# Kernel tuning notes

Measured on AMD Instinct MI355X. Metric: run time of the kernel, lower is better.

The kernel has to match this reference:

```python
import jax, jax.numpy as jnp
import numpy as np

B, C, H, W = 2, 512, 48, 48
HEADS, DHEAD = 8, 64
INNER = HEADS * DHEAD  # 512
CTX_LEN, CTX_DIM = 77, 768
FF_INNER = 4 * INNER   # 2048 (GEGLU inner dim)
GN_GROUPS, GN_EPS, LN_EPS = 32, 1e-6, 1e-5
SCALE = DHEAD ** -0.5


def setup_inputs() -> dict:
    key = jax.random.key(0)
    ks = iter(jax.random.split(key, 32))
    def nrm(shape, s=0.02):
        return jax.random.normal(next(ks), shape, jnp.float32) * s
    return dict(
        x=jax.random.normal(next(ks), (B, C, H, W), jnp.float32),
        context=jax.random.normal(next(ks), (B, CTX_LEN, CTX_DIM), jnp.float32),
        gn_g=jnp.ones((C,), jnp.float32), gn_b=jnp.zeros((C,), jnp.float32),
        w_in=nrm((C, INNER)), b_in=jnp.zeros((INNER,), jnp.float32),
        ln1_g=jnp.ones((INNER,), jnp.float32), ln1_b=jnp.zeros((INNER,), jnp.float32),
        wq1=nrm((INNER, INNER)), wk1=nrm((INNER, INNER)), wv1=nrm((INNER, INNER)),
        wo1=nrm((INNER, INNER)), bo1=jnp.zeros((INNER,), jnp.float32),
        ln2_g=jnp.ones((INNER,), jnp.float32), ln2_b=jnp.zeros((INNER,), jnp.float32),
        wq2=nrm((INNER, INNER)), wk2=nrm((CTX_DIM, INNER)), wv2=nrm((CTX_DIM, INNER)),
        wo2=nrm((INNER, INNER)), bo2=jnp.zeros((INNER,), jnp.float32),
        ln3_g=jnp.ones((INNER,), jnp.float32), ln3_b=jnp.zeros((INNER,), jnp.float32),
        w_ff1=nrm((INNER, 2 * FF_INNER)), b_ff1=jnp.zeros((2 * FF_INNER,), jnp.float32),
        w_ff2=nrm((FF_INNER, INNER)), b_ff2=jnp.zeros((INNER,), jnp.float32),
        w_out=nrm((INNER, C)), b_out=jnp.zeros((C,), jnp.float32),
    )


def _layernorm(x, g, b):
    m = jnp.mean(x, -1, keepdims=True)
    v = jnp.var(x, -1, keepdims=True)
    return (x - m) * jax.lax.rsqrt(v + LN_EPS) * g + b


def _groupnorm(x, g, b):
    bs, c, h, w = x.shape
    xg = x.reshape(bs, GN_GROUPS, c // GN_GROUPS, h, w)
    m = jnp.mean(xg, (2, 3, 4), keepdims=True)
    v = jnp.var(xg, (2, 3, 4), keepdims=True)
    xg = (xg - m) * jax.lax.rsqrt(v + GN_EPS)
    return xg.reshape(bs, c, h, w) * g[None, :, None, None] + b[None, :, None, None]


def _attn(x, ctx, wq, wk, wv, wo, bo):
    bs, n, _ = x.shape
    m = ctx.shape[1]
    q = (x @ wq).reshape(bs, n, HEADS, DHEAD).transpose(0, 2, 1, 3)    # b h n d
    k = (ctx @ wk).reshape(bs, m, HEADS, DHEAD).transpose(0, 2, 1, 3)  # b h m d
    v = (ctx @ wv).reshape(bs, m, HEADS, DHEAD).transpose(0, 2, 1, 3)
    sim = jnp.einsum('bhid,bhjd->bhij', q, k) * SCALE
    a = jax.nn.softmax(sim, axis=-1)
    o = jnp.einsum('bhij,bhjd->bhid', a, v)
    o = o.transpose(0, 2, 1, 3).reshape(bs, n, INNER)
    return o @ wo + bo


def reference(x, context, gn_g, gn_b, w_in, b_in,
              ln1_g, ln1_b, wq1, wk1, wv1, wo1, bo1,
              ln2_g, ln2_b, wq2, wk2, wv2, wo2, bo2,
              ln3_g, ln3_b, w_ff1, b_ff1, w_ff2, b_ff2,
              w_out, b_out):
    x_in = x
    h = _groupnorm(x, gn_g, gn_b)
    # proj_in: 1x1 conv == channel-wise linear
    h = jnp.einsum('bchw,cd->bdhw', h, w_in) + b_in[None, :, None, None]
    t = h.reshape(B, INNER, H * W).transpose(0, 2, 1)  # b n c
    # BasicTransformerBlock (depth=1)
    hn = _layernorm(t, ln1_g, ln1_b)
    t = _attn(hn, hn, wq1, wk1, wv1, wo1, bo1) + t          # self-attention
    hn = _layernorm(t, ln2_g, ln2_b)
    t = _attn(hn, context, wq2, wk2, wv2, wo2, bo2) + t     # cross-attention
    hn = _layernorm(t, ln3_g, ln3_b)
    u = hn @ w_ff1 + b_ff1                                   # GEGLU proj
    a_, g_ = jnp.split(u, 2, axis=-1)
    t = (a_ * jax.nn.gelu(g_, approximate=False)) @ w_ff2 + b_ff2 + t
    # back to image + proj_out 1x1 conv + residual
    y = t.transpose(0, 2, 1).reshape(B, INNER, H, W)
    y = jnp.einsum('bchw,cd->bdhw', y, w_out) + b_out[None, :, None, None]
    return y + x_in
```

## Files before the change

### kernel.cpp

```cpp
#include <hip/hip_runtime.h>
#include <hip/hip_bf16.h>

typedef __bf16 bf16_t;
typedef __bf16 bf16x4 __attribute__((ext_vector_type(4)));
typedef __bf16 bf16x8 __attribute__((ext_vector_type(8)));
typedef float f32x4 __attribute__((ext_vector_type(4)));

static __device__ __forceinline__ bf16x8 bzero8() {
  bf16x8 v;
#pragma unroll
  for (int j = 0; j < 8; j++) v[j] = (bf16_t)0.f;
  return v;
}

static __device__ __forceinline__ void async_copy16(const bf16_t* g, bf16_t* l) {
  __builtin_amdgcn_global_load_lds((const __attribute__((address_space(1))) void*)g,
                                   (__attribute__((address_space(3))) void*)l,
                                   16, 0, 0);
}
#define WAVE_LGKM() asm volatile("s_waitcnt lgkmcnt(0)" ::: "memory")

static __device__ __forceinline__ float fast_exp2(float x) {
  float r;
  asm volatile("v_exp_f32 %0, %1" : "=v"(r) : "v"(x));
  return r;
}

#define QK_SCALE 0.18033688f

__global__ void probe_kernel(const void* x, int* flag) {
  if (threadIdx.x != 0 || blockIdx.x != 0) return;
  const unsigned short* u = (const unsigned short*)x;
  int insane = 0;
  for (int j = 0; j < 512; j++) {
    unsigned short h = u[j];
    int e = (h >> 7) & 0xFF;
    if (e == 0xFF || e > 140 || (e != 0 && e < 100)) insane++;
  }
  *flag = (insane > 16) ? 1 : 0;
}

struct ConvArgs { const void* src[28]; int n[28]; int off[28]; };
__global__ __launch_bounds__(256) void convert_kernel(ConvArgs a, const int* flag,
                                                      bf16_t* dst) {
  int i = blockIdx.y;
  if (i >= 28) return;
  int n = a.n[i];
  if (n == 0) return;
  const void* s = a.src[i];
  bf16_t* d = dst + a.off[i];
  bool f32 = (*flag != 0);
  int n4 = n >> 2;
  for (int j = blockIdx.x * 256 + threadIdx.x; j < n4; j += gridDim.x * 256) {
    bf16x4 o;
    if (f32) {
      float4 v = ((const float4*)s)[j];
      o[0] = (bf16_t)v.x; o[1] = (bf16_t)v.y; o[2] = (bf16_t)v.z; o[3] = (bf16_t)v.w;
    } else {
      o = ((const bf16x4*)s)[j];
    }
    ((bf16x4*)d)[j] = o;
  }
  int base = n4 << 2;
  int j = base + blockIdx.x * 256 + threadIdx.x;
  if (j < n) {
    float v = f32 ? ((const float*)s)[j] : (float)((const bf16_t*)s)[j];
    d[j] = (bf16_t)v;
  }
}

struct TransArgs { const void* src[10]; int dst_off[10]; int K[10]; int N[10]; };
__global__ __launch_bounds__(256) void transpose_kernel(TransArgs ta, const int* flag,
                                                        bf16_t* __restrict__ wt) {
  int wi = blockIdx.y;
  int K = ta.K[wi], N = ta.N[wi];
  int tiles_n = N >> 6;
  int tile = blockIdx.x;
  if (tile >= tiles_n * (K >> 6)) return;
  int tk = tile / tiles_n, tn = tile - tk * tiles_n;
  int k0 = tk * 64, n0 = tn * 64;
  bf16_t* dst = wt + ta.dst_off[wi];
  bool f32 = (*flag != 0);
  __shared__ bf16_t tl[64][66];
  int t = threadIdx.x;
  int r = t >> 2, c = (t & 3) * 16;
  if (f32) {
    const float* src = (const float*)ta.src[wi] + (size_t)(k0 + r) * N + n0 + c;
#pragma unroll
    for (int q = 0; q < 4; q++) {
      float4 v = *(const float4*)(src + q * 4);
      tl[r][c + q * 4 + 0] = (bf16_t)v.x;
      tl[r][c + q * 4 + 1] = (bf16_t)v.y;
      tl[r][c + q * 4 + 2] = (bf16_t)v.z;
      tl[r][c + q * 4 + 3] = (bf16_t)v.w;
    }
  } else {
    const bf16_t* src = (const bf16_t*)ta.src[wi] + (size_t)(k0 + r) * N + n0 + c;
    bf16x8 v0 = *(const bf16x8*)(src);
    bf16x8 v1 = *(const bf16x8*)(src + 8);
#pragma unroll
    for (int j = 0; j < 8; j++) { tl[r][c + j] = v0[j]; tl[r][c + 8 + j] = v1[j]; }
  }
  __syncthreads();
  bf16x8 o0, o1;
#pragma unroll
  for (int j = 0; j < 8; j++) { o0[j] = tl[c + j][r]; o1[j] = tl[c + 8 + j][r]; }
  *(bf16x8*)(dst + (size_t)(n0 + r) * K + k0 + c) = o0;
  *(bf16x8*)(dst + (size_t)(n0 + r) * K + k0 + c + 8) = o1;
}

__global__ __launch_bounds__(256) void gn_stats_kernel(const bf16_t* __restrict__ x,
                                                       float* __restrict__ stats) {
  const bf16x8* base = (const bf16x8*)(x + (size_t)blockIdx.x * 36864);
  float s = 0.f, ss = 0.f;
  for (int i = threadIdx.x; i < 4608; i += 256) {
    bf16x8 v = base[i];
#pragma unroll
    for (int j = 0; j < 8; j++) { float f = (float)v[j]; s += f; ss += f * f; }
  }
  __shared__ float red[8];
#pragma unroll
  for (int off = 32; off > 0; off >>= 1) { s += __shfl_down(s, off); ss += __shfl_down(ss, off); }
  int wid = threadIdx.x >> 6;
  if ((threadIdx.x & 63) == 0) { red[wid] = s; red[4 + wid] = ss; }
  __syncthreads();
  if (threadIdx.x == 0) {
    float S = red[0] + red[1] + red[2] + red[3];
    float SS = red[4] + red[5] + red[6] + red[7];
    const float inv = 1.0f / 36864.0f;
    float mean = S * inv;
    float var = SS * inv - mean * mean;
    stats[blockIdx.x * 2] = mean;
    stats[blockIdx.x * 2 + 1] = rsqrtf(fmaxf(var, 0.f) + 1e-6f);
  }
}

__global__ __launch_bounds__(256) void gn_apply_kernel(const bf16_t* __restrict__ x,
                                                       const float* __restrict__ stats,
                                                       const bf16_t* __restrict__ g,
                                                       const bf16_t* __restrict__ bb,
                                                       bf16_t* __restrict__ xnt) {
  int p0 = blockIdx.x * 64, c0 = blockIdx.y * 64, bz = blockIdx.z;
  __shared__ bf16_t tl[64][66];
  int t = threadIdx.x;
  int r = t >> 2, cc = (t & 3) * 16;
  int c = c0 + r;
  float mean = stats[(bz * 32 + (c >> 4)) * 2];
  float rstd = stats[(bz * 32 + (c >> 4)) * 2 + 1];
  float gg = (float)g[c], bbv = (float)bb[c];
  const bf16_t* row = x + ((size_t)(bz * 512 + c)) * 2304 + p0 + cc;
  bf16x8 v0 = *(const bf16x8*)(row);
  bf16x8 v1 = *(const bf16x8*)(row + 8);
#pragma unroll
  for (int j = 0; j < 8; j++) {
    tl[r][cc + j] = (bf16_t)(((float)v0[j] - mean) * rstd * gg + bbv);
    tl[r][cc + 8 + j] = (bf16_t)(((float)v1[j] - mean) * rstd * gg + bbv);
  }
  __syncthreads();
  bf16x8 o0, o1;
#pragma unroll
  for (int j = 0; j < 8; j++) { o0[j] = tl[cc + j][r]; o1[j] = tl[cc + 8 + j][r]; }
  bf16_t* orow = xnt + ((size_t)(bz * 2304 + p0 + r)) * 512 + c0 + cc;
  *(bf16x8*)(orow) = o0;
  *(bf16x8*)(orow + 8) = o1;
}

__global__ __launch_bounds__(256) void ln_kernel(const float* __restrict__ in,
                                                 const bf16_t* __restrict__ g,
                                                 const bf16_t* __restrict__ b,
                                                 bf16_t* __restrict__ out) {
  int tok = blockIdx.x * 4 + (threadIdx.x >> 6);
  int lane = threadIdx.x & 63;
  const float* row = in + (size_t)tok * 512 + lane * 8;
  float f[8];
  float s = 0.f, ss = 0.f;
#pragma unroll
  for (int j = 0; j < 8; j++) { f[j] = row[j]; s += f[j]; ss += f[j] * f[j]; }
#pragma unroll
  for (int off = 32; off > 0; off >>= 1) { s += __shfl_xor(s, off); ss += __shfl_xor(ss, off); }
  float mean = s * (1.0f / 512.0f);
  float var = ss * (1.0f / 512.0f) - mean * mean;
  float rstd = rsqrtf(fmaxf(var, 0.f) + 1e-5f);
  bf16x8 gv = *(const bf16x8*)(g + lane * 8);
  bf16x8 bv = *(const bf16x8*)(b + lane * 8);
  bf16x8 o;
#pragma unroll
  for (int j = 0; j < 8; j++) o[j] = (bf16_t)((f[j] - mean) * rstd * (float)gv[j] + (float)bv[j]);
  *(bf16x8*)(out + (size_t)tok * 512 + lane * 8) = o;
}

template <int SMODE, int MODE>
__global__ __launch_bounds__(256) void gemm64d_kernel(
    const bf16_t* __restrict__ A, int lda,
    const bf16_t* __restrict__ Bt, int K, int N,
    const bf16_t* __restrict__ bias, float oscale,
    float* __restrict__ t32, bf16_t* __restrict__ C,
    const bf16_t* __restrict__ resb, const float* __restrict__ resf,
    float* __restrict__ Cf, const int* dflag) {
  __shared__ bf16_t As[2][4096];
  __shared__ bf16_t Bs[2][4096];
  int t = threadIdx.x, w = t >> 6, quad = (t >> 4) & 3, l16 = t & 15;
  int m0 = blockIdx.y * 64, n0 = blockIdx.x * 64;
  int wm = (w >> 1) * 32, wn = (w & 1) * 32;
  const f32x4 z4 = {0.f, 0.f, 0.f, 0.f};
  f32x4 acc[2][2] = {{z4, z4}, {z4, z4}};
  int r0 = t >> 3, c0 = ((t & 7) ^ (r0 & 7)) * 8;
  int r1 = r0 + 32, c1 = ((t & 7) ^ (r1 & 7)) * 8;
  const bf16_t* Ar0 = A + (size_t)(m0 + r0) * lda + c0;
  const bf16_t* Ar1 = A + (size_t)(m0 + r1) * lda + c1;
  const bf16_t* Br0 = Bt + (size_t)(n0 + r0) * K + c0;
  const bf16_t* Br1 = Bt + (size_t)(n0 + r1) * K + c1;
  int niter = K >> 6;
  async_copy16(Ar0, As[0] + w * 512);
  async_copy16(Ar1, As[0] + 2048 + w * 512);
  async_copy16(Br0, Bs[0] + w * 512);
  async_copy16(Br1, Bs[0] + 2048 + w * 512);
  for (int it = 0; it < niter; it++) {
    __syncthreads();
    if (it + 1 < niter) {
      int k0 = (it + 1) << 6;
      int nb = (it + 1) & 1;
      async_copy16(Ar0 + k0, As[nb] + w * 512);
      async_copy16(Ar1 + k0, As[nb] + 2048 + w * 512);
      async_copy16(Br0 + k0, Bs[nb] + w * 512);
      async_copy16(Br1 + k0, Bs[nb] + 2048 + w * 512);
    }
    int cb = it & 1;
    bf16x8 af[2][2], bff[2][2];
#pragma unroll
    for (int mi = 0; mi < 2; mi++) {
      int rr = wm + mi * 16 + l16;
      af[mi][0] = *(const bf16x8*)&As[cb][(rr * 8 + (quad ^ (rr & 7))) * 8];
      af[mi][1] = *(const bf16x8*)&As[cb][(rr * 8 + ((quad + 4) ^ (rr & 7))) * 8];
    }
#pragma unroll
    for (int ni = 0; ni < 2; ni++) {
      int rr = wn + ni * 16 + l16;
      bff[ni][0] = *(const bf16x8*)&Bs[cb][(rr * 8 + (quad ^ (rr & 7))) * 8];
      bff[ni][1] = *(const bf16x8*)&Bs[cb][(rr * 8 + ((quad + 4) ^ (rr & 7))) * 8];
    }
#pragma unroll
    for (int mi = 0; mi < 2; mi++)
#pragma unroll
      for (int ni = 0; ni < 2; ni++) {
        acc[mi][ni] = __builtin_amdgcn_mfma_f32_16x16x32_bf16(af[mi][0], bff[ni][0], acc[mi][ni], 0, 0, 0);
        acc[mi][ni] = __builtin_amdgcn_mfma_f32_16x16x32_bf16(af[mi][1], bff[ni][1], acc[mi][ni], 0, 0, 0);
      }
  }
  const bool f32m = (MODE == 3) && (*dflag != 0);
#pragma unroll
  for (int mi = 0; mi < 2; mi++)
#pragma unroll
    for (int ni = 0; ni < 2; ni++) {
      int col = n0 + wn + ni * 16 + l16;
      float bv = bias ? (float)bias[col] : 0.f;
#pragma unroll
      for (int r = 0; r < 4; r++) {
        int row = m0 + wm + mi * 16 + quad * 4 + r;
        float v = acc[mi][ni][r] + bv;
        size_t addr;
        if (SMODE == 0) {
          addr = (size_t)row * N + col;
        } else {
          int b2 = row / 2304; int p = row - b2 * 2304;
          addr = ((size_t)(b2 * 512 + col)) * 2304 + p;
        }
        if (MODE == 0) C[addr] = (bf16_t)(v * oscale);
        else if (MODE == 1) { t32[addr] = v; C[addr] = (bf16_t)v; }
        else if (MODE == 2) { v += t32[addr]; t32[addr] = v; C[addr] = (bf16_t)v; }
        else {
          v += f32m ? resf[addr] : (float)resb[addr];
          if (f32m) Cf[addr] = v; else C[addr] = (bf16_t)v;
        }
      }
    }
}

__global__ __launch_bounds__(256) void qkv3_kernel(
    const bf16_t* __restrict__ A,
    const bf16_t* __restrict__ BtQ, const bf16_t* __restrict__ BtK,
    const bf16_t* __restrict__ BtV,
    bf16_t* __restrict__ Qo, bf16_t* __restrict__ Ko, bf16_t* __restrict__ Vt) {
  __shared__ bf16_t As[2][4096];
  __shared__ bf16_t Bs[3][2][4096];
  int t = threadIdx.x, w = t >> 6, quad = (t >> 4) & 3, l16 = t & 15;
  int m0 = blockIdx.y * 64, n0 = blockIdx.x * 64;
  int wm = (w >> 1) * 32, wn = (w & 1) * 32;
  const f32x4 z4 = {0.f, 0.f, 0.f, 0.f};
  f32x4 acc[3][2][2];
#pragma unroll
  for (int z = 0; z < 3; z++)
#pragma unroll
    for (int mi = 0; mi < 2; mi++)
#pragma unroll
      for (int ni = 0; ni < 2; ni++) acc[z][mi][ni] = z4;
  int r0 = t >> 3, c0 = ((t & 7) ^ (r0 & 7)) * 8;
  int r1 = r0 + 32, c1 = ((t & 7) ^ (r1 & 7)) * 8;
  const bf16_t* Ar0 = A + (size_t)(m0 + r0) * 512 + c0;
  const bf16_t* Ar1 = A + (size_t)(m0 + r1) * 512 + c1;
  const bf16_t* Bw[3] = {BtQ, BtK, BtV};
  const bf16_t* Br0[3];
  const bf16_t* Br1[3];
#pragma unroll
  for (int z = 0; z < 3; z++) {
    Br0[z] = Bw[z] + (size_t)(n0 + r0) * 512 + c0;
    Br1[z] = Bw[z] + (size_t)(n0 + r1) * 512 + c1;
  }
  async_copy16(Ar0, As[0] + w * 512);
  async_copy16(Ar1, As[0] + 2048 + w * 512);
#pragma unroll
  for (int z = 0; z < 3; z++) {
    async_copy16(Br0[z], Bs[z][0] + w * 512);
    async_copy16(Br1[z], Bs[z][0] + 2048 + w * 512);
  }
  for (int it = 0; it < 8; it++) {
    __syncthreads();
    if (it + 1 < 8) {
      int k0 = (it + 1) << 6;
      int nb = (it + 1) & 1;
      async_copy16(Ar0 + k0, As[nb] + w * 512);
      async_copy16(Ar1 + k0, As[nb] + 2048 + w * 512);
#pragma unroll
      for (int z = 0; z < 3; z++) {
        async_copy16(Br0[z] + k0, Bs[z][nb] + w * 512);
        async_copy16(Br1[z] + k0, Bs[z][nb] + 2048 + w * 512);
      }
    }
    int cb = it & 1;
    bf16x8 af[2][2];
#pragma unroll
    for (int mi = 0; mi < 2; mi++) {
      int rr = wm + mi * 16 + l16;
      af[mi][0] = *(const bf16x8*)&As[cb][(rr * 8 + (quad ^ (rr & 7))) * 8];
      af[mi][1] = *(const bf16x8*)&As[cb][(rr * 8 + ((quad + 4) ^ (rr & 7))) * 8];
    }
#pragma unroll
    for (int z = 0; z < 3; z++) {
      bf16x8 bff[2][2];
#pragma unroll
      for (int ni = 0; ni < 2; ni++) {
        int rr = wn + ni * 16 + l16;
        bff[ni][0] = *(const bf16x8*)&Bs[z][cb][(rr * 8 + (quad ^ (rr & 7))) * 8];
        bff[ni][1] = *(const bf16x8*)&Bs[z][cb][(rr * 8 + ((quad + 4) ^ (rr & 7))) * 8];
      }
#pragma unroll
      for (int mi = 0; mi < 2; mi++)
#pragma unroll
        for (int ni = 0; ni < 2; ni++) {
          acc[z][mi][ni] = __builtin_amdgcn_mfma_f32_16x16x32_bf16(af[mi][0], bff[ni][0], acc[z][mi][ni], 0, 0, 0);
          acc[z][mi][ni] = __builtin_amdgcn_mfma_f32_16x16x32_bf16(af[mi][1], bff[ni][1], acc[z][mi][ni], 0, 0, 0);
        }
    }
  }
#pragma unroll
  for (int mi = 0; mi < 2; mi++)
#pragma unroll
    for (int ni = 0; ni < 2; ni++) {
      int col = n0 + wn + ni * 16 + l16;
#pragma unroll
      for (int r = 0; r < 4; r++) {
        int row = m0 + wm + mi * 16 + quad * 4 + r;
        Qo[(size_t)row * 512 + col] = (bf16_t)(acc[0][mi][ni][r] * QK_SCALE);
        Ko[(size_t)row * 512 + col] = (bf16_t)acc[1][mi][ni][r];
        int b2 = row / 2304; int p = row - b2 * 2304;
        Vt[((size_t)(b2 * 512 + col)) * 2304 + p] = (bf16_t)acc[2][mi][ni][r];
      }
    }
}

__global__ __launch_bounds__(256) void ff1_kernel(const bf16_t* __restrict__ A,
                                                  const bf16_t* __restrict__ Bt,
                                                  const bf16_t* __restrict__ bias,
                                                  bf16_t* __restrict__ U) {
  __shared__ bf16_t As[2][4096];
  __shared__ bf16_t Ba[2][4096];
  __shared__ bf16_t Bg[2][4096];
  int t = threadIdx.x, w = t >> 6, quad = (t >> 4) & 3, l16 = t & 15;
  int m0 = blockIdx.y * 64, n0 = blockIdx.x * 64;
  int wm = (w >> 1) * 32, wn = (w & 1) * 32;
  const f32x4 z4 = {0.f, 0.f, 0.f, 0.f};
  f32x4 aa[2][2] = {{z4, z4}, {z4, z4}};
  f32x4 ag[2][2] = {{z4, z4}, {z4, z4}};
  int r0 = t >> 3, c0 = ((t & 7) ^ (r0 & 7)) * 8;
  int r1 = r0 + 32, c1 = ((t & 7) ^ (r1 & 7)) * 8;
  const bf16_t* Ar0 = A + (size_t)(m0 + r0) * 512 + c0;
  const bf16_t* Ar1 = A + (size_t)(m0 + r1) * 512 + c1;
  const bf16_t* Ba0 = Bt + (size_t)(n0 + r0) * 512 + c0;
  const bf16_t* Ba1 = Bt + (size_t)(n0 + r1) * 512 + c1;
  const bf16_t* Bg0 = Bt + (size_t)(2048 + n0 + r0) * 512 + c0;
  const bf16_t* Bg1 = Bt + (size_t)(2048 + n0 + r1) * 512 + c1;
  async_copy16(Ar0, As[0] + w * 512);
  async_copy16(Ar1, As[0] + 2048 + w * 512);
  async_copy16(Ba0, Ba[0] + w * 512);
  async_copy16(Ba1, Ba[0] + 2048 + w * 512);
  async_copy16(Bg0, Bg[0] + w * 512);
  async_copy16(Bg1, Bg[0] + 2048 + w * 512);
  for (int it = 0; it < 8; it++) {
    __syncthreads();
    if (it + 1 < 8) {
      int k0 = (it + 1) << 6;
      int nb = (it + 1) & 1;
      async_copy16(Ar0 + k0, As[nb] + w * 512);
      async_copy16(Ar1 + k0, As[nb] + 2048 + w * 512);
      async_copy16(Ba0 + k0, Ba[nb] + w * 512);
      async_copy16(Ba1 + k0, Ba[nb] + 2048 + w * 512);
      async_copy16(Bg0 + k0, Bg[nb] + w * 512);
      async_copy16(Bg1 + k0, Bg[nb] + 2048 + w * 512);
    }
    int cb = it & 1;
    bf16x8 af[2][2], ba[2][2], bg[2][2];
#pragma unroll
    for (int mi = 0; mi < 2; mi++) {
      int rr = wm + mi * 16 + l16;
      af[mi][0] = *(const bf16x8*)&As[cb][(rr * 8 + (quad ^ (rr & 7))) * 8];
      af[mi][1] = *(const bf16x8*)&As[cb][(rr * 8 + ((quad + 4) ^ (rr & 7))) * 8];
    }
#pragma unroll
    for (int ni = 0; ni < 2; ni++) {
      int rr = wn + ni * 16 + l16;
      int o0 = (rr * 8 + (quad ^ (rr & 7))) * 8;
      int o1 = (rr * 8 + ((quad + 4) ^ (rr & 7))) * 8;
      ba[ni][0] = *(const bf16x8*)&Ba[cb][o0];
      ba[ni][1] = *(const bf16x8*)&Ba[cb][o1];
      bg[ni][0] = *(const bf16x8*)&Bg[cb][o0];
      bg[ni][1] = *(const bf16x8*)&Bg[cb][o1];
    }
#pragma unroll
    for (int mi = 0; mi < 2; mi++)
#pragma unroll
      for (int ni = 0; ni < 2; ni++) {
        aa[mi][ni] = __builtin_amdgcn_mfma_f32_16x16x32_bf16(af[mi][0], ba[ni][0], aa[mi][ni], 0, 0, 0);
        aa[mi][ni] = __builtin_amdgcn_mfma_f32_16x16x32_bf16(af[mi][1], ba[ni][1], aa[mi][ni], 0, 0, 0);
        ag[mi][ni] = __builtin_amdgcn_mfma_f32_16x16x32_bf16(af[mi][0], bg[ni][0], ag[mi][ni], 0, 0, 0);
        ag[mi][ni] = __builtin_amdgcn_mfma_f32_16x16x32_bf16(af[mi][1], bg[ni][1], ag[mi][ni], 0, 0, 0);
      }
  }
#pragma unroll
  for (int mi = 0; mi < 2; mi++)
#pragma unroll
    for (int ni = 0; ni < 2; ni++) {
      int col = n0 + wn + ni * 16 + l16;
      float bba = (float)bias[col], bbg = (float)bias[col + 2048];
#pragma unroll
      for (int r = 0; r < 4; r++) {
        int row = m0 + wm + mi * 16 + quad * 4 + r;
        float a = aa[mi][ni][r] + bba;
        float g = ag[mi][ni][r] + bbg;
        float gl = 0.5f * g * (1.0f + erff(g * 0.70710678118654752f));
        U[(size_t)row * 2048 + col] = (bf16_t)(a * gl);
      }
    }
}

__global__ __launch_bounds__(256) void kv2_kernel(const bf16_t* __restrict__ A,
                                                  const bf16_t* __restrict__ Bk,
                                                  const bf16_t* __restrict__ Bv,
                                                  bf16_t* __restrict__ Ck,
                                                  bf16_t* __restrict__ Cv) {
  const int M = 154, N = 512, K = 768;
  int z = blockIdx.z;
  const bf16_t* B = z ? Bv : Bk;
  __shared__ alignas(16) bf16_t As[64][40];
  __shared__ alignas(16) bf16_t Bs[64][40];
  int t = threadIdx.x;
  int m0 = blockIdx.y * 64, n0 = blockIdx.x * 64;
  int w = t >> 6, lane = t & 63, quad = lane >> 4, l16 = lane & 15;
  int ar = t >> 2, ac = (t & 3) * 8;
  int br = t >> 3, bc = (t & 7) * 8;
  const f32x4 z4 = {0.f, 0.f, 0.f, 0.f};
  f32x4 acc[4] = {z4, z4, z4, z4};
  int gm = m0 + ar;
  const bool a_ok = gm < M;
  for (int k0 = 0; k0 < K; k0 += 32) {
    bf16x8 av = a_ok ? *(const bf16x8*)(A + (size_t)gm * K + k0 + ac) : bzero8();
    bf16x8 bv = *(const bf16x8*)(B + (size_t)(k0 + br) * N + n0 + bc);
    __syncthreads();
    *(bf16x8*)(&As[ar][ac]) = av;
#pragma unroll
    for (int j = 0; j < 8; j++) Bs[bc + j][br] = bv[j];
    __syncthreads();
    bf16x8 afrag = *(const bf16x8*)(&As[w * 16 + l16][quad * 8]);
#pragma unroll
    for (int kb = 0; kb < 4; kb++) {
      bf16x8 bfrag = *(const bf16x8*)(&Bs[kb * 16 + l16][quad * 8]);
      acc[kb] = __builtin_amdgcn_mfma_f32_16x16x32_bf16(afrag, bfrag, acc[kb], 0, 0, 0);
    }
  }
#pragma unroll
  for (int kb = 0; kb < 4; kb++) {
    int col = n0 + kb * 16 + l16;
#pragma unroll
    for (int r = 0; r < 4; r++) {
      int row = m0 + w * 16 + quad * 4 + r;
      if (row < M) {
        float v = acc[kb][r];
        if (z == 0) Ck[(size_t)row * N + col] = (bf16_t)v;
        else {
          int b2 = row / 77; int p = row - b2 * 77;
          Cv[((size_t)(b2 * 512 + col)) * 128 + p] = (bf16_t)v;
        }
      }
    }
  }
}

template <bool MASK>
__global__ __launch_bounds__(128) void flash6_kernel(const bf16_t* __restrict__ q,
                                                     const bf16_t* __restrict__ kk,
                                                     const bf16_t* __restrict__ vt,
                                                     bf16_t* __restrict__ out,
                                                     int n_k, int kv_bstride, int vt_len) {
  __shared__ bf16_t Ks[2][4096];
  __shared__ bf16_t Vs[2][4096];
  __shared__ bf16_t p_lds[2][32 * 72];
  int t = threadIdx.x, w = t >> 6, quad = (t >> 4) & 3, l16 = t & 15;
  int b = blockIdx.y >> 3, h = blockIdx.y & 7;
  int q0 = blockIdx.x * 64 + w * 32;
  bf16x8 qa[2][2];
#pragma unroll
  for (int si = 0; si < 2; si++) {
    const bf16_t* qrow = q + ((size_t)(b * 2304 + q0 + si * 16 + l16)) * 512 + h * 64 + quad * 8;
    qa[si][0] = *(const bf16x8*)(qrow);
    qa[si][1] = *(const bf16x8*)(qrow + 32);
  }
  const f32x4 z4 = {0.f, 0.f, 0.f, 0.f};
  f32x4 o[2][4];
  float l_i[2] = {0.f, 0.f};
#pragma unroll
  for (int si = 0; si < 2; si++)
#pragma unroll
    for (int db = 0; db < 4; db++) o[si][db] = z4;
  const bf16_t* kbase = kk + (size_t)b * kv_bstride + h * 64;
  const bf16_t* vbase = vt + ((size_t)((b * 8 + h) * 64)) * vt_len;
  int kr[4], kc[4];
#pragma unroll
  for (int i = 0; i < 4; i++) {
    int g = t + 128 * i;
    kr[i] = g >> 3;
    kc[i] = ((g & 7) ^ (kr[i] & 7)) * 8;
  }
  int n_kt = (n_k + 63) >> 6;
#pragma unroll
  for (int i = 0; i < 4; i++) {
    async_copy16(kbase + (size_t)kr[i] * 512 + kc[i], Ks[0] + w * 512 + i * 1024);
    async_copy16(vbase + (size_t)kr[i] * vt_len + kc[i], Vs[0] + w * 512 + i * 1024);
  }
  for (int kt = 0; kt < n_kt; kt++) {
    int kc0 = kt * 64;
    __syncthreads();
    if (kt + 1 < n_kt) {
      int kn = (kt + 1) * 64;
      int nb = (kt + 1) & 1;
#pragma unroll
      for (int i = 0; i < 4; i++) {
        async_copy16(kbase + (size_t)(kn + kr[i]) * 512 + kc[i], Ks[nb] + w * 512 + i * 1024);
        async_copy16(vbase + (size_t)kr[i] * vt_len + kn + kc[i], Vs[nb] + w * 512 + i * 1024);
      }
    }
    int cb = kt & 1;
    bf16x8 kf[4][2], vf[4][2];
#pragma unroll
    for (int kb = 0; kb < 4; kb++) {
      int rr = kb * 16 + l16;
#pragma unroll
      for (int c = 0; c < 2; c++) {
        int gi = (rr * 8 + ((quad + c * 4) ^ (rr & 7))) * 8;
        kf[kb][c] = *(const bf16x8*)&Ks[cb][gi];
        vf[kb][c] = *(const bf16x8*)&Vs[cb][gi];
      }
    }
#pragma unroll
    for (int si = 0; si < 2; si++) {
      f32x4 s[4] = {z4, z4, z4, z4};
#pragma unroll
      for (int kb = 0; kb < 4; kb++) {
        s[kb] = __builtin_amdgcn_mfma_f32_16x16x32_bf16(kf[kb][0], qa[si][0], s[kb], 0, 0, 0);
        s[kb] = __builtin_amdgcn_mfma_f32_16x16x32_bf16(kf[kb][1], qa[si][1], s[kb], 0, 0, 0);
      }
      float rs = 0.f;
#pragma unroll
      for (int kb = 0; kb < 4; kb++)
#pragma unroll
        for (int r = 0; r < 4; r++) {
          float sv = s[kb][r];
          if (MASK && (kc0 + kb * 16 + quad * 4 + r) >= n_k) sv = -1e30f;
          float pp = fast_exp2(sv);
          s[kb][r] = pp;
          rs += pp;
        }
      rs += __shfl_xor(rs, 16);
      rs += __shfl_xor(rs, 32);
      l_i[si] += rs;
      WAVE_LGKM();
#pragma unroll
      for (int kb = 0; kb < 4; kb++) {
        bf16x4 pk;
#pragma unroll
        for (int r = 0; r < 4; r++) pk[r] = (bf16_t)s[kb][r];
        *(bf16x4*)&p_lds[w][(si * 16 + l16) * 72 + kb * 16 + quad * 4] = pk;
      }
      WAVE_LGKM();
      bf16x8 pa0 = *(const bf16x8*)&p_lds[w][(si * 16 + l16) * 72 + quad * 8];
      bf16x8 pa1 = *(const bf16x8*)&p_lds[w][(si * 16 + l16) * 72 + 32 + quad * 8];
#pragma unroll
      for (int db = 0; db < 4; db++) {
        o[si][db] = __builtin_amdgcn_mfma_f32_16x16x32_bf16(vf[db][0], pa0, o[si][db], 0, 0, 0);
        o[si][db] = __builtin_amdgcn_mfma_f32_16x16x32_bf16(vf[db][1], pa1, o[si][db], 0, 0, 0);
      }
    }
  }
#pragma unroll
  for (int si = 0; si < 2; si++) {
    float inv = 1.0f / l_i[si];
    bf16_t* orow = out + ((size_t)(b * 2304 + q0 + si * 16 + l16)) * 512 + h * 64 + quad * 4;
#pragma unroll
    for (int db = 0; db < 4; db++) {
      bf16x4 pk;
#pragma unroll
      for (int r = 0; r < 4; r++) pk[r] = (bf16_t)(o[si][db][r] * inv);
      *(bf16x4*)(orow + db * 16) = pk;
    }
  }
}

extern "C" void kernel_launch(void* const* d_in, const int* in_sizes, int n_in,
                              void* d_out, int out_size, void* d_ws, size_t ws_size,
                              hipStream_t stream) {
  (void)out_size; (void)ws_size;
  char* p = (char*)d_ws;
  int* flag = (int*)p;
  float* stats = (float*)(p + 16);
  float* t32 = (float*)(p + 1024);
  const size_t TOK512 = (size_t)4608 * 512;
  bf16_t* conv = (bf16_t*)(p + 1024 + TOK512 * 4);

  const int widx[10] = {4, 8, 9, 10, 11, 15, 18, 22, 24, 26};
  const int wK[10] = {512, 512, 512, 512, 512, 512, 512, 512, 2048, 512};
  const int wN[10] = {512, 512, 512, 512, 512, 512, 512, 4096, 512, 512};
  bool is_wt[28] = {};
  for (int i = 0; i < 10; i++) is_wt[widx[i]] = true;

  ConvArgs ca;
  int off = 0;
  int noff[28];
  for (int i = 0; i < 28; i++) {
    ca.src[i] = (i < n_in) ? d_in[i] : nullptr;
    ca.n[i] = (i < n_in && !is_wt[i]) ? in_sizes[i] : 0;
    ca.off[i] = off;
    noff[i] = off;
    int sz = (i < n_in) ? in_sizes[i] : 0;
    off += ((is_wt[i] ? 0 : sz) + 7) & ~7;
  }
  bf16_t* wt = conv + ((off + 7) & ~7);
  TransArgs ta;
  int woff = 0, wtoff[10];
  for (int i = 0; i < 10; i++) {
    ta.src[i] = d_in[widx[i]];
    ta.dst_off[i] = woff;
    wtoff[i] = woff;
    ta.K[i] = wK[i]; ta.N[i] = wN[i];
    woff += wK[i] * wN[i];
  }
  bf16_t* hn  = wt + woff;
  bf16_t* tb  = hn + TOK512;
  bf16_t* xnt = tb + TOK512;
  bf16_t* qb  = xnt + TOK512;
  bf16_t* kbuf = qb + TOK512;
  bf16_t* vtb = kbuf + TOK512;
  bf16_t* ub2 = xnt;
  bf16_t* ob  = xnt;

  const bf16_t* xb    = conv + noff[0];
  const bf16_t* ctxb  = conv + noff[1];
  const bf16_t* gn_g  = conv + noff[2];
  const bf16_t* gn_b  = conv + noff[3];
  const bf16_t* b_in  = conv + noff[5];
  const bf16_t* ln1_g = conv + noff[6];
  const bf16_t* ln1_b = conv + noff[7];
  const bf16_t* bo1   = conv + noff[12];
  const bf16_t* ln2_g = conv + noff[13];
  const bf16_t* ln2_b = conv + noff[14];
  const bf16_t* wk2   = conv + noff[16];
  const bf16_t* wv2   = conv + noff[17];
  const bf16_t* bo2   = conv + noff[19];
  const bf16_t* ln3_g = conv + noff[20];
  const bf16_t* ln3_b = conv + noff[21];
  const bf16_t* b_ff1 = conv + noff[23];
  const bf16_t* b_ff2 = conv + noff[25];
  const bf16_t* b_out = conv + noff[27];
  const bf16_t* wt_in  = wt + wtoff[0];
  const bf16_t* wt_q1  = wt + wtoff[1];
  const bf16_t* wt_k1  = wt + wtoff[2];
  const bf16_t* wt_v1  = wt + wtoff[3];
  const bf16_t* wt_o1  = wt + wtoff[4];
  const bf16_t* wt_q2  = wt + wtoff[5];
  const bf16_t* wt_o2  = wt + wtoff[6];
  const bf16_t* wt_ff1 = wt + wtoff[7];
  const bf16_t* wt_ff2 = wt + wtoff[8];
  const bf16_t* wt_out = wt + wtoff[9];

  probe_kernel<<<1, 64, 0, stream>>>(d_in[0], flag);
  convert_kernel<<<dim3(128, 28), 256, 0, stream>>>(ca, flag, conv);
  transpose_kernel<<<dim3(512, 10), 256, 0, stream>>>(ta, flag, wt);

  gn_stats_kernel<<<64, 256, 0, stream>>>(xb, stats);
  gn_apply_kernel<<<dim3(36, 8, 2), 256, 0, stream>>>(xb, stats, gn_g, gn_b, xnt);
  gemm64d_kernel<0, 1><<<dim3(8, 72), 256, 0, stream>>>(xnt, 512, wt_in, 512, 512, b_in, 1.f, t32, tb, nullptr, nullptr, nullptr, nullptr);
  ln_kernel<<<1152, 256, 0, stream>>>(t32, ln1_g, ln1_b, hn);
  qkv3_kernel<<<dim3(8, 72), 256, 0, stream>>>(hn, wt_q1, wt_k1, wt_v1, qb, kbuf, vtb);
  flash6_kernel<false><<<dim3(36, 16), 128, 0, stream>>>(qb, kbuf, vtb, ob, 2304, 2304 * 512, 2304);
  gemm64d_kernel<0, 2><<<dim3(8, 72), 256, 0, stream>>>(ob, 512, wt_o1, 512, 512, bo1, 1.f, t32, tb, nullptr, nullptr, nullptr, nullptr);
  ln_kernel<<<1152, 256, 0, stream>>>(t32, ln2_g, ln2_b, hn);
  gemm64d_kernel<0, 0><<<dim3(8, 72), 256, 0, stream>>>(hn, 512, wt_q2, 512, 512, nullptr, QK_SCALE, nullptr, qb, nullptr, nullptr, nullptr, nullptr);
  kv2_kernel<<<dim3(8, 3, 2), 256, 0, stream>>>(ctxb, wk2, wv2, kbuf, vtb);
  flash6_kernel<true><<<dim3(36, 16), 128, 0, stream>>>(qb, kbuf, vtb, ob, 77, 77 * 512, 128);
  gemm64d_kernel<0, 2><<<dim3(8, 72), 256, 0, stream>>>(ob, 512, wt_o2, 512, 512, bo2, 1.f, t32, tb, nullptr, nullptr, nullptr, nullptr);
  ln_kernel<<<1152, 256, 0, stream>>>(t32, ln3_g, ln3_b, hn);
  ff1_kernel<<<dim3(32, 72), 256, 0, stream>>>(hn, wt_ff1, b_ff1, ub2);
  gemm64d_kernel<0, 2><<<dim3(8, 72), 256, 0, stream>>>(ub2, 2048, wt_ff2, 2048, 512, b_ff2, 1.f, t32, tb, nullptr, nullptr, nullptr, nullptr);
  gemm64d_kernel<1, 3><<<dim3(8, 72), 256, 0, stream>>>(tb, 512, wt_out, 512, 512, b_out, 1.f, nullptr, (bf16_t*)d_out, xb, (const float*)d_in[0], (float*)d_out, flag);
}
```

Baseline: 411.1 us.

## Split self-attention keys across blocks and enlarge GEGLU FF1 tiles to 128x128

Self-attention now splits the 2304 keys into three chunks handled by separate blocks of four 16-row waves. Each block writes fp32 partial outputs and row sums, and a new reduce kernel combines them and normalizes. This raises parallelism and occupancy, at the cost of extra fp32 traffic and one more launch. The FF1 GEGLU kernel also moves to 128x128 tiles with K-steps of 32, for more register reuse per load but fewer blocks.

```diff
diff --git a/kernel.cpp b/kernel.cpp
--- a/kernel.cpp
+++ b/kernel.cpp
@@ -27,6 +27,7 @@
 }
 
 #define QK_SCALE 0.18033688f
+#define TOKC ((size_t)4608 * 512)
 
 __global__ void probe_kernel(const void* x, int* flag) {
   if (threadIdx.x != 0 || blockIdx.x != 0) return;
@@ -376,13 +377,17 @@
   __shared__ bf16_t Ba[2][4096];
   __shared__ bf16_t Bg[2][4096];
   int t = threadIdx.x, w = t >> 6, quad = (t >> 4) & 3, l16 = t & 15;
-  int m0 = blockIdx.y * 64, n0 = blockIdx.x * 64;
-  int wm = (w >> 1) * 32, wn = (w & 1) * 32;
+  int m0 = blockIdx.y * 128, n0 = blockIdx.x * 128;
+  int wm = (w >> 1) * 64, wn = (w & 1) * 64;
   const f32x4 z4 = {0.f, 0.f, 0.f, 0.f};
-  f32x4 aa[2][2] = {{z4, z4}, {z4, z4}};
-  f32x4 ag[2][2] = {{z4, z4}, {z4, z4}};
-  int r0 = t >> 3, c0 = ((t & 7) ^ (r0 & 7)) * 8;
-  int r1 = r0 + 32, c1 = ((t & 7) ^ (r1 & 7)) * 8;
+  f32x4 aa[4][4], gg[4][4];
+#pragma unroll
+  for (int i = 0; i < 4; i++)
+#pragma unroll
+    for (int j = 0; j < 4; j++) { aa[i][j] = z4; gg[i][j] = z4; }
+  int r0 = t >> 2, c0 = ((t & 3) ^ (r0 & 3)) * 8;
+  int g1 = t + 256;
+  int r1 = g1 >> 2, c1 = ((g1 & 3) ^ (r1 & 3)) * 8;
   const bf16_t* Ar0 = A + (size_t)(m0 + r0) * 512 + c0;
   const bf16_t* Ar1 = A + (size_t)(m0 + r1) * 512 + c1;
   const bf16_t* Ba0 = Bt + (size_t)(n0 + r0) * 512 + c0;
@@ -395,10 +400,10 @@
   async_copy16(Ba1, Ba[0] + 2048 + w * 512);
   async_copy16(Bg0, Bg[0] + w * 512);
   async_copy16(Bg1, Bg[0] + 2048 + w * 512);
-  for (int it = 0; it < 8; it++) {
+  for (int it = 0; it < 16; it++) {
     __syncthreads();
-    if (it + 1 < 8) {
-      int k0 = (it + 1) << 6;
+    if (it + 1 < 16) {
+      int k0 = (it + 1) << 5;
       int nb = (it + 1) & 1;
       async_copy16(Ar0 + k0, As[nb] + w * 512);
       async_copy16(Ar1 + k0, As[nb] + 2048 + w * 512);
@@ -408,44 +413,38 @@
       async_copy16(Bg1 + k0, Bg[nb] + 2048 + w * 512);
     }
     int cb = it & 1;
-    bf16x8 af[2][2], ba[2][2], bg[2][2];
-#pragma unroll
-    for (int mi = 0; mi < 2; mi++) {
+    bf16x8 af[4], ba[4], bg[4];
+#pragma unroll
+    for (int mi = 0; mi < 4; mi++) {
       int rr = wm + mi * 16 + l16;
-      af[mi][0] = *(const bf16x8*)&As[cb][(rr * 8 + (quad ^ (rr & 7))) * 8];
-      af[mi][1] = *(const bf16x8*)&As[cb][(rr * 8 + ((quad + 4) ^ (rr & 7))) * 8];
-    }
-#pragma unroll
-    for (int ni = 0; ni < 2; ni++) {
+      af[mi] = *(const bf16x8*)&As[cb][(rr * 4 + (quad ^ (rr & 3))) * 8];
+    }
+#pragma unroll
+    for (int ni = 0; ni < 4; ni++) {
       int rr = wn + ni * 16 + l16;
-      int o0 = (rr * 8 + (quad ^ (rr & 7))) * 8;
-      int o1 = (rr * 8 + ((quad + 4) ^ (rr & 7))) * 8;
-      ba[ni][0] = *(const bf16x8*)&Ba[cb][o0];
-      ba[ni][1] = *(const bf16x8*)&Ba[cb][o1];
-      bg[ni][0] = *(const bf16x8*)&Bg[cb][o0];
-      bg[ni][1] = *(const bf16x8*)&Bg[cb][o1];
-    }
-#pragma unroll
-    for (int mi = 0; mi < 2; mi++)
-#pragma unroll
-      for (int ni = 0; ni < 2; ni++) {
-        aa[mi][ni] = __builtin_amdgcn_mfma_f32_16x16x32_bf16(af[mi][0], ba[ni][0], aa[mi][ni], 0, 0, 0);
-        aa[mi][ni] = __builtin_amdgcn_mfma_f32_16x16x32_bf16(af[mi][1], ba[ni][1], aa[mi][ni], 0, 0, 0);
-        ag[mi][ni] = __builtin_amdgcn_mfma_f32_16x16x32_bf16(af[mi][0], bg[ni][0], ag[mi][ni], 0, 0, 0);
-        ag[mi][ni] = __builtin_amdgcn_mfma_f32_16x16x32_bf16(af[mi][1], bg[ni][1], ag[mi][ni], 0, 0, 0);
-      }
-  }
-#pragma unroll
-  for (int mi = 0; mi < 2; mi++)
-#pragma unroll
-    for (int ni = 0; ni < 2; ni++) {
+      int off = (rr * 4 + (quad ^ (rr & 3))) * 8;
+      ba[ni] = *(const bf16x8*)&Ba[cb][off];
+      bg[ni] = *(const bf16x8*)&Bg[cb][off];
+    }
+#pragma unroll
+    for (int mi = 0; mi < 4; mi++)
+#pragma unroll
+      for (int ni = 0; ni < 4; ni++) {
+        aa[mi][ni] = __builtin_amdgcn_mfma_f32_16x16x32_bf16(af[mi], ba[ni], aa[mi][ni], 0, 0, 0);
+        gg[mi][ni] = __builtin_amdgcn_mfma_f32_16x16x32_bf16(af[mi], bg[ni], gg[mi][ni], 0, 0, 0);
+      }
+  }
+#pragma unroll
+  for (int mi = 0; mi < 4; mi++)
+#pragma unroll
+    for (int ni = 0; ni < 4; ni++) {
       int col = n0 + wn + ni * 16 + l16;
       float bba = (float)bias[col], bbg = (float)bias[col + 2048];
 #pragma unroll
       for (int r = 0; r < 4; r++) {
         int row = m0 + wm + mi * 16 + quad * 4 + r;
         float a = aa[mi][ni][r] + bba;
-        float g = ag[mi][ni][r] + bbg;
+        float g = gg[mi][ni][r] + bbg;
         float gl = 0.5f * g * (1.0f + erff(g * 0.70710678118654752f));
         U[(size_t)row * 2048 + col] = (bf16_t)(a * gl);
       }
@@ -504,58 +503,47 @@
   }
 }
 
-template <bool MASK>
-__global__ __launch_bounds__(128) void flash6_kernel(const bf16_t* __restrict__ q,
+template <int KSPLIT, bool MASK>
+__global__ __launch_bounds__(256) void flash7_kernel(const bf16_t* __restrict__ q,
                                                      const bf16_t* __restrict__ kk,
                                                      const bf16_t* __restrict__ vt,
                                                      bf16_t* __restrict__ out,
+                                                     float* __restrict__ Of,
+                                                     float* __restrict__ lp,
                                                      int n_k, int kv_bstride, int vt_len) {
   __shared__ bf16_t Ks[2][4096];
   __shared__ bf16_t Vs[2][4096];
-  __shared__ bf16_t p_lds[2][32 * 72];
+  __shared__ bf16_t p_lds[4][16 * 72];
   int t = threadIdx.x, w = t >> 6, quad = (t >> 4) & 3, l16 = t & 15;
   int b = blockIdx.y >> 3, h = blockIdx.y & 7;
-  int q0 = blockIdx.x * 64 + w * 32;
-  bf16x8 qa[2][2];
-#pragma unroll
-  for (int si = 0; si < 2; si++) {
-    const bf16_t* qrow = q + ((size_t)(b * 2304 + q0 + si * 16 + l16)) * 512 + h * 64 + quad * 8;
-    qa[si][0] = *(const bf16x8*)(qrow);
-    qa[si][1] = *(const bf16x8*)(qrow + 32);
-  }
+  int s = (KSPLIT > 1) ? blockIdx.z : 0;
+  int chunk = n_k / KSPLIT;
+  int q0 = blockIdx.x * 64 + w * 16;
+  const bf16_t* qrow = q + ((size_t)(b * 2304 + q0 + l16)) * 512 + h * 64 + quad * 8;
+  bf16x8 qa0 = *(const bf16x8*)(qrow);
+  bf16x8 qa1 = *(const bf16x8*)(qrow + 32);
   const f32x4 z4 = {0.f, 0.f, 0.f, 0.f};
-  f32x4 o[2][4];
-  float l_i[2] = {0.f, 0.f};
-#pragma unroll
-  for (int si = 0; si < 2; si++)
-#pragma unroll
-    for (int db = 0; db < 4; db++) o[si][db] = z4;
-  const bf16_t* kbase = kk + (size_t)b * kv_bstride + h * 64;
-  const bf16_t* vbase = vt + ((size_t)((b * 8 + h) * 64)) * vt_len;
-  int kr[4], kc[4];
-#pragma unroll
-  for (int i = 0; i < 4; i++) {
-    int g = t + 128 * i;
-    kr[i] = g >> 3;
-    kc[i] = ((g & 7) ^ (kr[i] & 7)) * 8;
-  }
-  int n_kt = (n_k + 63) >> 6;
-#pragma unroll
-  for (int i = 0; i < 4; i++) {
-    async_copy16(kbase + (size_t)kr[i] * 512 + kc[i], Ks[0] + w * 512 + i * 1024);
-    async_copy16(vbase + (size_t)kr[i] * vt_len + kc[i], Vs[0] + w * 512 + i * 1024);
-  }
+  f32x4 o[4] = {z4, z4, z4, z4};
+  float l_i = 0.f;
+  const bf16_t* kbase = kk + (size_t)b * kv_bstride + h * 64 + (size_t)s * chunk * 512;
+  const bf16_t* vbase = vt + ((size_t)((b * 8 + h) * 64)) * vt_len + s * chunk;
+  int kr0 = t >> 3, kc0g = ((t & 7) ^ (kr0 & 7)) * 8;
+  int kr1 = kr0 + 32, kc1g = ((t & 7) ^ (kr1 & 7)) * 8;
+  int n_kt = (chunk + 63) >> 6;
+  async_copy16(kbase + (size_t)kr0 * 512 + kc0g, Ks[0] + w * 512);
+  async_copy16(kbase + (size_t)kr1 * 512 + kc1g, Ks[0] + 2048 + w * 512);
+  async_copy16(vbase + (size_t)kr0 * vt_len + kc0g, Vs[0] + w * 512);
+  async_copy16(vbase + (size_t)kr1 * vt_len + kc1g, Vs[0] + 2048 + w * 512);
   for (int kt = 0; kt < n_kt; kt++) {
     int kc0 = kt * 64;
     __syncthreads();
     if (kt + 1 < n_kt) {
       int kn = (kt + 1) * 64;
       int nb = (kt + 1) & 1;
-#pragma unroll
-      for (int i = 0; i < 4; i++) {
-        async_copy16(kbase + (size_t)(kn + kr[i]) * 512 + kc[i], Ks[nb] + w * 512 + i * 1024);
-        async_copy16(vbase + (size_t)kr[i] * vt_len + kn + kc[i], Vs[nb] + w * 512 + i * 1024);
-      }
+      async_copy16(kbase + (size_t)(kn + kr0) * 512 + kc0g, Ks[nb] + w * 512);
+      async_copy16(kbase + (size_t)(kn + kr1) * 512 + kc1g, Ks[nb] + 2048 + w * 512);
+      async_copy16(vbase + (size_t)kr0 * vt_len + kn + kc0g, Vs[nb] + w * 512);
+      async_copy16(vbase + (size_t)kr1 * vt_len + kn + kc1g, Vs[nb] + 2048 + w * 512);
     }
     int cb = kt & 1;
     bf16x8 kf[4][2], vf[4][2];
@@ -569,58 +557,86 @@
         vf[kb][c] = *(const bf16x8*)&Vs[cb][gi];
       }
     }
-#pragma unroll
-    for (int si = 0; si < 2; si++) {
-      f32x4 s[4] = {z4, z4, z4, z4};
-#pragma unroll
-      for (int kb = 0; kb < 4; kb++) {
-        s[kb] = __builtin_amdgcn_mfma_f32_16x16x32_bf16(kf[kb][0], qa[si][0], s[kb], 0, 0, 0);
-        s[kb] = __builtin_amdgcn_mfma_f32_16x16x32_bf16(kf[kb][1], qa[si][1], s[kb], 0, 0, 0);
-      }
-      float rs = 0.f;
-#pragma unroll
-      for (int kb = 0; kb < 4; kb++)
-#pragma unroll
-        for (int r = 0; r < 4; r++) {
-          float sv = s[kb][r];
-          if (MASK && (kc0 + kb * 16 + quad * 4 + r) >= n_k) sv = -1e30f;
-          float pp = fast_exp2(sv);
-          s[kb][r] = pp;
-          rs += pp;
-        }
-      rs += __shfl_xor(rs, 16);
-      rs += __shfl_xor(rs, 32);
-      l_i[si] += rs;
-      WAVE_LGKM();
-#pragma unroll
-      for (int kb = 0; kb < 4; kb++) {
-        bf16x4 pk;
-#pragma unroll
-        for (int r = 0; r < 4; r++) pk[r] = (bf16_t)s[kb][r];
-        *(bf16x4*)&p_lds[w][(si * 16 + l16) * 72 + kb * 16 + quad * 4] = pk;
-      }
-      WAVE_LGKM();
-      bf16x8 pa0 = *(const bf16x8*)&p_lds[w][(si * 16 + l16) * 72 + quad * 8];
-      bf16x8 pa1 = *(const bf16x8*)&p_lds[w][(si * 16 + l16) * 72 + 32 + quad * 8];
-#pragma unroll
-      for (int db = 0; db < 4; db++) {
-        o[si][db] = __builtin_amdgcn_mfma_f32_16x16x32_bf16(vf[db][0], pa0, o[si][db], 0, 0, 0);
-        o[si][db] = __builtin_amdgcn_mfma_f32_16x16x32_bf16(vf[db][1], pa1, o[si][db], 0, 0, 0);
-      }
-    }
-  }
-#pragma unroll
-  for (int si = 0; si < 2; si++) {
-    float inv = 1.0f / l_i[si];
-    bf16_t* orow = out + ((size_t)(b * 2304 + q0 + si * 16 + l16)) * 512 + h * 64 + quad * 4;
+    f32x4 sx[4] = {z4, z4, z4, z4};
+#pragma unroll
+    for (int kb = 0; kb < 4; kb++) {
+      sx[kb] = __builtin_amdgcn_mfma_f32_16x16x32_bf16(kf[kb][0], qa0, sx[kb], 0, 0, 0);
+      sx[kb] = __builtin_amdgcn_mfma_f32_16x16x32_bf16(kf[kb][1], qa1, sx[kb], 0, 0, 0);
+    }
+    float rs = 0.f;
+#pragma unroll
+    for (int kb = 0; kb < 4; kb++)
+#pragma unroll
+      for (int r = 0; r < 4; r++) {
+        float sv = sx[kb][r];
+        if (MASK && (kc0 + kb * 16 + quad * 4 + r) >= n_k) sv = -1e30f;
+        float pp = fast_exp2(sv);
+        sx[kb][r] = pp;
+        rs += pp;
+      }
+    rs += __shfl_xor(rs, 16);
+    rs += __shfl_xor(rs, 32);
+    l_i += rs;
+    WAVE_LGKM();
+#pragma unroll
+    for (int kb = 0; kb < 4; kb++) {
+      bf16x4 pk;
+#pragma unroll
+      for (int r = 0; r < 4; r++) pk[r] = (bf16_t)sx[kb][r];
+      *(bf16x4*)&p_lds[w][l16 * 72 + kb * 16 + quad * 4] = pk;
+    }
+    WAVE_LGKM();
+    bf16x8 pa0 = *(const bf16x8*)&p_lds[w][l16 * 72 + quad * 8];
+    bf16x8 pa1 = *(const bf16x8*)&p_lds[w][l16 * 72 + 32 + quad * 8];
+#pragma unroll
+    for (int db = 0; db < 4; db++) {
+      o[db] = __builtin_amdgcn_mfma_f32_16x16x32_bf16(vf[db][0], pa0, o[db], 0, 0, 0);
+      o[db] = __builtin_amdgcn_mfma_f32_16x16x32_bf16(vf[db][1], pa1, o[db], 0, 0, 0);
+    }
+  }
+  if (KSPLIT == 1) {
+    float inv = 1.0f / l_i;
+    bf16_t* orow = out + ((size_t)(b * 2304 + q0 + l16)) * 512 + h * 64 + quad * 4;
 #pragma unroll
     for (int db = 0; db < 4; db++) {
       bf16x4 pk;
 #pragma unroll
-      for (int r = 0; r < 4; r++) pk[r] = (bf16_t)(o[si][db][r] * inv);
+      for (int r = 0; r < 4; r++) pk[r] = (bf16_t)(o[db][r] * inv);
       *(bf16x4*)(orow + db * 16) = pk;
     }
-  }
+  } else {
+    float* orowf = Of + (size_t)s * TOKC + ((size_t)(b * 2304 + q0 + l16)) * 512 + h * 64 + quad * 4;
+#pragma unroll
+    for (int db = 0; db < 4; db++) *(f32x4*)(orowf + db * 16) = o[db];
+    if ((t & 63) < 16)
+      lp[(size_t)s * 4608 * 8 + ((size_t)(b * 2304 + q0 + l16)) * 8 + h] = l_i;
+  }
+}
+
+__global__ __launch_bounds__(256) void att_reduce_kernel(const float* __restrict__ Of,
+                                                         const float* __restrict__ lp,
+                                                         bf16_t* __restrict__ out) {
+  size_t idx = (size_t)blockIdx.x * 256 + threadIdx.x;
+  size_t base = idx * 8;
+  int row = (int)(base >> 9);
+  int col = (int)(base & 511);
+  int h = col >> 6;
+  size_t li = (size_t)row * 8 + h;
+  float ls = lp[li] + lp[4608 * 8 + li] + lp[2 * 4608 * 8 + li];
+  float inv = 1.0f / ls;
+  f32x4 a0 = *(const f32x4*)(Of + base);
+  f32x4 a1 = *(const f32x4*)(Of + base + 4);
+  f32x4 b0 = *(const f32x4*)(Of + TOKC + base);
+  f32x4 b1 = *(const f32x4*)(Of + TOKC + base + 4);
+  f32x4 c0 = *(const f32x4*)(Of + 2 * TOKC + base);
+  f32x4 c1 = *(const f32x4*)(Of + 2 * TOKC + base + 4);
+  bf16x8 o;
+#pragma unroll
+  for (int j = 0; j < 4; j++) {
+    o[j] = (bf16_t)((a0[j] + b0[j] + c0[j]) * inv);
+    o[4 + j] = (bf16_t)((a1[j] + b1[j] + c1[j]) * inv);
+  }
+  *(bf16x8*)(out + base) = o;
 }
 
 extern "C" void kernel_launch(void* const* d_in, const int* in_sizes, int n_in,
@@ -631,8 +647,7 @@
   int* flag = (int*)p;
   float* stats = (float*)(p + 16);
   float* t32 = (float*)(p + 1024);
-  const size_t TOK512 = (size_t)4608 * 512;
-  bf16_t* conv = (bf16_t*)(p + 1024 + TOK512 * 4);
+  bf16_t* conv = (bf16_t*)(p + 1024 + TOKC * 4);
 
   const int widx[10] = {4, 8, 9, 10, 11, 15, 18, 22, 24, 26};
   const int wK[10] = {512, 512, 512, 512, 512, 512, 512, 512, 2048, 512};
@@ -662,11 +677,13 @@
     woff += wK[i] * wN[i];
   }
   bf16_t* hn  = wt + woff;
-  bf16_t* tb  = hn + TOK512;
-  bf16_t* xnt = tb + TOK512;
-  bf16_t* qb  = xnt + TOK512;
-  bf16_t* kbuf = qb + TOK512;
-  bf16_t* vtb = kbuf + TOK512;
+  bf16_t* tb  = hn + TOKC;
+  bf16_t* xnt = tb + TOKC;
+  bf16_t* qb  = xnt + TOKC;
+  bf16_t* kbuf = qb + TOKC;
+  bf16_t* vtb = kbuf + TOKC;
+  float*  Opart = (float*)(vtb + TOKC);
+  float*  lpart = Opart + 3 * TOKC;
   bf16_t* ub2 = xnt;
   bf16_t* ob  = xnt;
 
@@ -708,15 +725,16 @@
   gemm64d_kernel<0, 1><<<dim3(8, 72), 256, 0, stream>>>(xnt, 512, wt_in, 512, 512, b_in, 1.f, t32, tb, nullptr, nullptr, nullptr, nullptr);
   ln_kernel<<<1152, 256, 0, stream>>>(t32, ln1_g, ln1_b, hn);
   qkv3_kernel<<<dim3(8, 72), 256, 0, stream>>>(hn, wt_q1, wt_k1, wt_v1, qb, kbuf, vtb);
-  flash6_kernel<false><<<dim3(36, 16), 128, 0, stream>>>(qb, kbuf, vtb, ob, 2304, 2304 * 512, 2304);
+  flash7_kernel<3, false><<<dim3(36, 16, 3), 256, 0, stream>>>(qb, kbuf, vtb, ob, Opart, lpart, 2304, 2304 * 512, 2304);
+  att_reduce_kernel<<<1152, 256, 0, stream>>>(Opart, lpart, ob);
   gemm64d_kernel<0, 2><<<dim3(8, 72), 256, 0, stream>>>(ob, 512, wt_o1, 512, 512, bo1, 1.f, t32, tb, nullptr, nullptr, nullptr, nullptr);
   ln_kernel<<<1152, 256, 0, stream>>>(t32, ln2_g, ln2_b, hn);
   gemm64d_kernel<0, 0><<<dim3(8, 72), 256, 0, stream>>>(hn, 512, wt_q2, 512, 512, nullptr, QK_SCALE, nullptr, qb, nullptr, nullptr, nullptr, nullptr);
   kv2_kernel<<<dim3(8, 3, 2), 256, 0, stream>>>(ctxb, wk2, wv2, kbuf, vtb);
-  flash6_kernel<true><<<dim3(36, 16), 128, 0, stream>>>(qb, kbuf, vtb, ob, 77, 77 * 512, 128);
+  flash7_kernel<1, true><<<dim3(36, 16, 1), 256, 0, stream>>>(qb, kbuf, vtb, ob, nullptr, nullptr, 77, 77 * 512, 128);
   gemm64d_kernel<0, 2><<<dim3(8, 72), 256, 0, stream>>>(ob, 512, wt_o2, 512, 512, bo2, 1.f, t32, tb, nullptr, nullptr, nullptr, nullptr);
   ln_kernel<<<1152, 256, 0, stream>>>(t32, ln3_g, ln3_b, hn);
-  ff1_kernel<<<dim3(32, 72), 256, 0, stream>>>(hn, wt_ff1, b_ff1, ub2);
+  ff1_kernel<<<dim3(16, 36), 256, 0, stream>>>(hn, wt_ff1, b_ff1, ub2);
   gemm64d_kernel<0, 2><<<dim3(8, 72), 256, 0, stream>>>(ub2, 2048, wt_ff2, 2048, 512, b_ff2, 1.f, t32, tb, nullptr, nullptr, nullptr, nullptr);
   gemm64d_kernel<1, 3><<<dim3(8, 72), 256, 0, stream>>>(tb, 512, wt_out, 512, 512, b_out, 1.f, nullptr, (bf16_t*)d_out, xb, (const float*)d_in[0], (float*)d_out, flag);
 }
```

New measurement: 429.6 us. 1.05x slower.
